# Performance work log

Hardware: AMD Instinct MI355X
Metric: run time of the kernel (lower is better)

The kernel has to match this reference:

```python
import jax, jax.numpy as jnp
import numpy as np

B, C_IN, C_OUT, H, W = 4, 256, 256, 64, 64
K, STRIDE, PAD, DIL = 3, 1, 1, 1
KK = K * K


def setup_inputs() -> dict:
    key = jax.random.key(0)
    k1, k2, k3, k4 = jax.random.split(key, 4)
    x = jax.random.normal(k1, (B, C_IN, H, W), jnp.float32)
    # offset/mask conv weight (no bias), scaled small so offsets are modest
    w_mod = jax.random.normal(k2, (3 * KK, C_IN, K, K), jnp.float32) * 0.01
    # deform conv weight (xavier-ish scale) + bias
    w_def = jax.random.normal(k3, (C_OUT, C_IN, K, K), jnp.float32) * (1.0 / np.sqrt(C_IN * KK))
    b_def = jax.random.normal(k4, (C_OUT,), jnp.float32) * 0.01
    return {"x": x, "w_mod": w_mod, "w_def": w_def, "b_def": b_def}


def _conv_nchw(x, w, stride, pad):
    return jax.lax.conv_general_dilated(
        x, w, (stride, stride), [(pad, pad), (pad, pad)],
        dimension_numbers=("NCHW", "OIHW", "NCHW"))


def _bilinear_sample(x, py, px):
    # x: [B,C,H,W]; py/px: [B,KK,Ho,Wo] absolute sample coords (zero-pad outside)
    Bn, Cc, Hh, Ww = x.shape
    y0 = jnp.floor(py)
    x0 = jnp.floor(px)
    fy = py - y0
    fx = px - x0
    y0i = y0.astype(jnp.int32)
    x0i = x0.astype(jnp.int32)
    xf = x.reshape(Bn, Cc, Hh * Ww)

    def corner(yi, xi, wgt):
        valid = (yi >= 0) & (yi < Hh) & (xi >= 0) & (xi < Ww)
        yc = jnp.clip(yi, 0, Hh - 1)
        xc = jnp.clip(xi, 0, Ww - 1)
        idx = yc * Ww + xc                      # [B,KK,Ho,Wo]
        g = jax.vmap(lambda f, i: f[:, i])(xf, idx)  # [B,C,KK,Ho,Wo]
        return g * (wgt * valid)[:, None]

    return (corner(y0i, x0i, (1 - fy) * (1 - fx))
            + corner(y0i, x0i + 1, (1 - fy) * fx)
            + corner(y0i + 1, x0i, fy * (1 - fx))
            + corner(y0i + 1, x0i + 1, fy * fx))


def reference(x, w_mod, w_def, b_def):
    # offset/mask head
    mod = _conv_nchw(x, w_mod, STRIDE, PAD)          # [B, 3*KK, Ho, Wo]
    o1, o2, mask = mod[:, :KK], mod[:, KK:2 * KK], mod[:, 2 * KK:]
    offset = jnp.concatenate([o1, o2], axis=1)        # [B, 2*KK, Ho, Wo]
    # torchvision DeformConv2d: offset channels are interleaved (y, x) pairs
    dy = offset[:, 0::2]
    dx = offset[:, 1::2]
    mask = jax.nn.sigmoid(mask)                       # [B, KK, Ho, Wo]

    Ho, Wo = mod.shape[2], mod.shape[3]
    ky, kx = jnp.meshgrid(jnp.arange(K), jnp.arange(K), indexing="ij")
    ky = ky.reshape(-1).astype(jnp.float32)
    kx = kx.reshape(-1).astype(jnp.float32)
    base_y = (jnp.arange(Ho, dtype=jnp.float32) * STRIDE - PAD)[None, :, None] + (ky * DIL)[:, None, None]  # [KK,Ho,1]
    base_x = (jnp.arange(Wo, dtype=jnp.float32) * STRIDE - PAD)[None, None, :] + (kx * DIL)[:, None, None]  # [KK,1,Wo]
    py = dy + base_y[None]                            # [B,KK,Ho,Wo]
    px = dx + base_x[None]

    sampled = _bilinear_sample(x, py, px) * mask[:, None]  # [B,C,KK,Ho,Wo]
    out = jnp.einsum("bckhw,ock->bohw", sampled, w_def.reshape(C_OUT, C_IN, KK))
    return out + b_def[None, :, None, None]
```

## Files before the change

kernel.cpp:

```cpp
#include <hip/hip_runtime.h>

typedef unsigned short u16;
typedef unsigned int u32;
typedef short bf16x8 __attribute__((ext_vector_type(8)));
typedef float f32x4 __attribute__((ext_vector_type(4)));

#define CIN 256
#define COUT 256

__device__ __forceinline__ u16 f2b(float f) {
  u32 u = __float_as_uint(f);
  u += 0x7fffu + ((u >> 16) & 1u);
  return (u16)(u >> 16);
}
__device__ __forceinline__ u32 packbf(float lo, float hi) {
  return (u32)f2b(lo) | ((u32)f2b(hi) << 16);
}
__device__ __forceinline__ u32 bil2(u32 u00, u32 u01, u32 u10, u32 u11, float4 wt) {
  float s0 = __uint_as_float(u00 << 16) * wt.x;
  s0 = fmaf(__uint_as_float(u01 << 16), wt.y, s0);
  s0 = fmaf(__uint_as_float(u10 << 16), wt.z, s0);
  s0 = fmaf(__uint_as_float(u11 << 16), wt.w, s0);
  float s1 = __uint_as_float(u00 & 0xffff0000u) * wt.x;
  s1 = fmaf(__uint_as_float(u01 & 0xffff0000u), wt.y, s1);
  s1 = fmaf(__uint_as_float(u10 & 0xffff0000u), wt.z, s1);
  s1 = fmaf(__uint_as_float(u11 & 0xffff0000u), wt.w, s1);
  return packbf(s0, s1);
}
__device__ __forceinline__ void bar() {
  asm volatile("s_waitcnt lgkmcnt(0)\n\ts_barrier" ::: "memory");
}

__global__ __launch_bounds__(256) void k_prep(
    const float* __restrict__ x, const float* __restrict__ w_mod,
    const float* __restrict__ w_def,
    u16* __restrict__ xT, u16* __restrict__ Wm2, u16* __restrict__ W2) {
  __shared__ __align__(16) char SB[9216];
  int t = threadIdx.x, g = blockIdx.x;
  if (g < 1024) {
    u16 (*T)[72] = (u16(*)[72])SB;
    int b = g >> 8, ct = (g >> 6) & 3, pt = g & 63;
    int c0 = ct << 6, pos0 = pt << 6;
    {
      int cl = t >> 2, pb = (t & 3) << 4;
      const float* p = x + (((b << 8) + c0 + cl) << 12) + pos0 + pb;
#pragma unroll
      for (int i = 0; i < 4; ++i) {
        float4 v = *(const float4*)(p + i * 4);
        int pp = pb + i * 4;
        T[pp][cl] = f2b(v.x); T[pp + 1][cl] = f2b(v.y);
        T[pp + 2][cl] = f2b(v.z); T[pp + 3][cl] = f2b(v.w);
      }
    }
    __syncthreads();
    {
      int pl = t >> 2, q = t & 3;
      u16* dst = xT + (((b << 12) + pos0 + pl) << 8) + c0 + (q << 4);
      *(uint4*)dst = *(const uint4*)&T[pl][q << 4];
      *(uint4*)(dst + 8) = *(const uint4*)&T[pl][(q << 4) + 8];
    }
  } else {
    float* L = (float*)SB;
    int gg = g - 1024;
    if (gg < 256) {
      const float* src = w_def + gg * 2304;
      for (int j = t; j < 2304; j += 256) L[j] = src[j];
      __syncthreads();
      u16* dst = W2 + gg * 2304;
      for (int j = t; j < 2304; j += 256) {
        int kk = j >> 8, c = j & 255;
        dst[j] = f2b(L[c * 9 + kk]);
      }
    } else {
      int cm = gg - 256;
      if (cm < 27) {
        const float* src = w_mod + cm * 2304;
        for (int j = t; j < 2304; j += 256) L[j] = src[j];
      }
      __syncthreads();
      u16* dst = Wm2 + cm * 2304;
      for (int j = t; j < 2304; j += 256) {
        int kk = j >> 8, c = j & 255;
        dst[j] = (cm < 27) ? f2b(L[c * 9 + kk]) : (u16)0;
      }
    }
  }
}

__global__ __launch_bounds__(512) void k_modconv(
    const u16* __restrict__ xT, const u16* __restrict__ Wm2,
    int2* __restrict__ cidx, float4* __restrict__ cwt) {
  __shared__ __align__(16) u16 As[2][2][64][72];
  __shared__ float mods2[2][32][66];
  int t = threadIdx.x;
  int l = t & 63;
  int w = t >> 6;
  int h = t >> 8;
  int wl = w & 3;
  int tg = t & 255;
  int px = tg >> 2, q = tg & 3;
  int g = blockIdx.x;
  int b = (g & 7) >> 1, y = ((g >> 3) << 1) + (g & 1);
  const u16* xTb = xT + (b << 20);
  f32x4 zero = {0.f, 0.f, 0.f, 0.f};
  f32x4 acc0 = zero, acc1 = zero;
  int ml = l & 15, kq = l >> 4;

  uint4 VA0, VA1, VB0, VB1;
  uint4 S0, S1, S2, S3, T0, T1, T2, T3;

#define MC_ISSUE_A(i, V0, V1)                                                \
  { int ch_ = h * 18 + (i); int kk_ = ch_ >> 2, c0_ = (ch_ & 3) << 6;        \
    int ky_ = kk_ / 3, kx_ = kk_ - 3 * ky_;                                  \
    int ys_ = y + ky_ - 1, xs_ = px + kx_ - 1;                               \
    V0 = make_uint4(0, 0, 0, 0); V1 = V0;                                    \
    if (ys_ >= 0 && ys_ < 64 && xs_ >= 0 && xs_ < 64) {                      \
      const u16* p_ = xTb + (((ys_ << 6) + xs_) << 8) + c0_ + (q << 4);      \
      V0 = *(const uint4*)p_; V1 = *(const uint4*)(p_ + 8);                  \
    } }

#define MC_ISSUE_B(i, R0, R1, R2, R3)                                        \
  { int ch_ = h * 18 + (i); int kk_ = ch_ >> 2, c0_ = (ch_ & 3) << 6;        \
    const u16* pw_ = Wm2 + (kk_ << 8) + c0_ + (kq << 3);                     \
    R0 = *(const uint4*)(pw_ + ml * 2304);                                   \
    R1 = *(const uint4*)(pw_ + (16 + ml) * 2304);                            \
    R2 = *(const uint4*)(pw_ + ml * 2304 + 32);                              \
    R3 = *(const uint4*)(pw_ + (16 + ml) * 2304 + 32); }

#define MC_WRITE(buf, V0, V1)                                                \
  { *(uint4*)&As[h][buf][px][q << 4] = V0;                                   \
    *(uint4*)&As[h][buf][px][(q << 4) + 8] = V1; }

#define MC_MFMA(buf, R0, R1, R2, R3)                                         \
  { bf16x8 a0_ = *(const bf16x8*)&As[h][buf][wl * 16 + ml][kq << 3];         \
    acc0 = __builtin_amdgcn_mfma_f32_16x16x32_bf16(a0_, *(const bf16x8*)&R0, acc0, 0,0,0); \
    acc1 = __builtin_amdgcn_mfma_f32_16x16x32_bf16(a0_, *(const bf16x8*)&R1, acc1, 0,0,0); \
    bf16x8 a1_ = *(const bf16x8*)&As[h][buf][wl * 16 + ml][32 + (kq << 3)];  \
    acc0 = __builtin_amdgcn_mfma_f32_16x16x32_bf16(a1_, *(const bf16x8*)&R2, acc0, 0,0,0); \
    acc1 = __builtin_amdgcn_mfma_f32_16x16x32_bf16(a1_, *(const bf16x8*)&R3, acc1, 0,0,0); }

  MC_ISSUE_A(0, VA0, VA1)
  MC_ISSUE_A(1, VB0, VB1)
  MC_ISSUE_B(0, S0, S1, S2, S3)
#pragma unroll 1
  for (int i2 = 0; i2 < 18; i2 += 2) {
    MC_WRITE(0, VA0, VA1)
    bar();
    if (i2 + 2 < 18) MC_ISSUE_A(i2 + 2, VA0, VA1)
    MC_ISSUE_B(i2 + 1, T0, T1, T2, T3)
    MC_MFMA(0, S0, S1, S2, S3)
    MC_WRITE(1, VB0, VB1)
    bar();
    if (i2 + 3 < 18) MC_ISSUE_A(i2 + 3, VB0, VB1)
    if (i2 + 2 < 18) MC_ISSUE_B(i2 + 2, S0, S1, S2, S3)
    MC_MFMA(1, T0, T1, T2, T3)
  }
#pragma unroll
  for (int r = 0; r < 4; ++r) {
    mods2[h][ml][wl * 16 + kq * 4 + r]      = acc0[r];
    mods2[h][16 + ml][wl * 16 + kq * 4 + r] = acc1[r];
  }
  __syncthreads();
  for (int i2 = t; i2 < 576; i2 += 512) {
    int kk = i2 >> 6, pxx_i = i2 & 63;
    float dy = mods2[0][2 * kk][pxx_i] + mods2[1][2 * kk][pxx_i];
    float dx = mods2[0][2 * kk + 1][pxx_i] + mods2[1][2 * kk + 1][pxx_i];
    float mv = mods2[0][18 + kk][pxx_i] + mods2[1][18 + kk][pxx_i];
    float msk = 1.f / (1.f + __expf(-mv));
    int ky = kk / 3, kx = kk - 3 * ky;
    float py  = dy + (float)(y + ky - 1);
    float pxx = dx + (float)(pxx_i + kx - 1);
    float y0f = floorf(py), x0f = floorf(pxx);
    float fy = py - y0f, fx = pxx - x0f;
    int y0 = (int)y0f, x0 = (int)x0f;
    float vy0 = (y0 >= 0 && y0 < 64) ? msk : 0.f;
    float vy1 = (y0 + 1 >= 0 && y0 + 1 < 64) ? msk : 0.f;
    float w00 = (1.f - fy) * (1.f - fx) * vy0;
    float w01 = (1.f - fy) * fx * vy0;
    float w10 = fy * (1.f - fx) * vy1;
    float w11 = fy * fx * vy1;
    int xb2 = min(max(x0, 0), 62);
    float wA0 = (xb2 == x0) ? w00 : ((xb2 == x0 + 1) ? w01 : 0.f);
    float wB0 = (xb2 + 1 == x0) ? w00 : ((xb2 + 1 == x0 + 1) ? w01 : 0.f);
    float wA1 = (xb2 == x0) ? w10 : ((xb2 == x0 + 1) ? w11 : 0.f);
    float wB1 = (xb2 + 1 == x0) ? w10 : ((xb2 + 1 == x0 + 1) ? w11 : 0.f);
    int ib0 = min(max(y0, 0), 63) * 64 + xb2;
    int ib1 = min(max(y0 + 1, 0), 63) * 64 + xb2;
    int ci = ((b * 9 + kk) << 12) + (y << 6) + pxx_i;
    cidx[ci] = make_int2(ib0, ib1);
    cwt[ci]  = make_float4(wA0, wB0, wA1, wB1);
  }
#undef MC_ISSUE_A
#undef MC_ISSUE_B
#undef MC_WRITE
#undef MC_MFMA
}

__global__ __launch_bounds__(512) void k_main(
    const u16* __restrict__ xT, const u16* __restrict__ W2,
    const float* __restrict__ b_def,
    const int2* __restrict__ cidx, const float4* __restrict__ cwt,
    float* __restrict__ out) {
  __shared__ __align__(16) u16 As[2][64][72];
  __shared__ __align__(16) int2 Cs_i[576];
  __shared__ __align__(16) float4 Cs_w[576];
  int t = threadIdx.x;
  int l = t & 63;
  int w = t >> 6;
  int g = blockIdx.x;
  int b = (g & 7) >> 1, y = ((g >> 3) << 1) + (g & 1);
  const u16* xTb = xT + (b << 20);
  int gm = t >> 3, go = t & 7;
  int ml = l & 15, kq = l >> 4;
  int nrow0 = w * 32 + ml, nrow1 = nrow0 + 16;

  f32x4 zero = {0.f, 0.f, 0.f, 0.f};
  f32x4 acc[4][2];
#pragma unroll
  for (int i = 0; i < 4; ++i) { acc[i][0] = zero; acc[i][1] = zero; }

  for (int i = t; i < 576; i += 512) {
    int kk = i >> 6, px = i & 63;
    int ci = ((b * 9 + kk) << 12) + (y << 6) + px;
    Cs_i[i] = cidx[ci];
    Cs_w[i] = cwt[ci];
  }
  bar();

  uint4 A00, A01, A02, A03; float4 wt0;
  uint4 A10, A11, A12, A13; float4 wt1;
  uint4 RA0, RA1, RA2, RA3;
  uint4 RB0, RB1, RB2, RB3;

#define ISSUE_A(chunk, a0, a1, a2, a3, wt)                                   \
  { int kk_ = (chunk) >> 2, c0_ = ((chunk) & 3) << 6;                        \
    int cI_ = (kk_ << 6) + gm;                                               \
    int2 ib_ = Cs_i[cI_];                                                    \
    wt = Cs_w[cI_];                                                          \
    const u16* p0_ = xTb + (ib_.x << 8) + c0_ + (go << 3);                   \
    const u16* p1_ = xTb + (ib_.y << 8) + c0_ + (go << 3);                   \
    a0 = *(const uint4*)p0_;  a1 = *(const uint4*)(p0_ + 256);               \
    a2 = *(const uint4*)p1_;  a3 = *(const uint4*)(p1_ + 256); }

#define ISSUE_B(chunk, R0, R1, R2, R3)                                       \
  { int kk_ = (chunk) >> 2, c0_ = ((chunk) & 3) << 6;                        \
    const u16* pw_ = W2 + (kk_ << 8) + c0_ + (kq << 3);                      \
    R0 = *(const uint4*)(pw_ + nrow0 * 2304);                                \
    R1 = *(const uint4*)(pw_ + nrow1 * 2304);                                \
    R2 = *(const uint4*)(pw_ + nrow0 * 2304 + 32);                           \
    R3 = *(const uint4*)(pw_ + nrow1 * 2304 + 32); }

#define UNPACK(CUR, a0, a1, a2, a3, wt)                                      \
  { u32 q0_ = bil2(a0.x, a1.x, a2.x, a3.x, wt);                              \
    u32 q1_ = bil2(a0.y, a1.y, a2.y, a3.y, wt);                              \
    u32 q2_ = bil2(a0.z, a1.z, a2.z, a3.z, wt);                              \
    u32 q3_ = bil2(a0.w, a1.w, a2.w, a3.w, wt);                              \
    *(uint4*)&As[CUR][gm][go << 3] = make_uint4(q0_, q1_, q2_, q3_); }

#define DOMFMA(CUR, R0, R1, R2, R3)                                          \
  { bf16x8 a0_ = *(const bf16x8*)&As[CUR][ml][kq << 3];                      \
    bf16x8 a1_ = *(const bf16x8*)&As[CUR][16 + ml][kq << 3];                 \
    bf16x8 a2_ = *(const bf16x8*)&As[CUR][32 + ml][kq << 3];                 \
    bf16x8 a3_ = *(const bf16x8*)&As[CUR][48 + ml][kq << 3];                 \
    bf16x8 b0_ = *(const bf16x8*)&R0;                                        \
    bf16x8 b1_ = *(const bf16x8*)&R1;                                        \
    acc[0][0] = __builtin_amdgcn_mfma_f32_16x16x32_bf16(a0_, b0_, acc[0][0], 0,0,0); \
    acc[1][0] = __builtin_amdgcn_mfma_f32_16x16x32_bf16(a1_, b0_, acc[1][0], 0,0,0); \
    acc[2][0] = __builtin_amdgcn_mfma_f32_16x16x32_bf16(a2_, b0_, acc[2][0], 0,0,0); \
    acc[3][0] = __builtin_amdgcn_mfma_f32_16x16x32_bf16(a3_, b0_, acc[3][0], 0,0,0); \
    acc[0][1] = __builtin_amdgcn_mfma_f32_16x16x32_bf16(a0_, b1_, acc[0][1], 0,0,0); \
    acc[1][1] = __builtin_amdgcn_mfma_f32_16x16x32_bf16(a1_, b1_, acc[1][1], 0,0,0); \
    acc[2][1] = __builtin_amdgcn_mfma_f32_16x16x32_bf16(a2_, b1_, acc[2][1], 0,0,0); \
    acc[3][1] = __builtin_amdgcn_mfma_f32_16x16x32_bf16(a3_, b1_, acc[3][1], 0,0,0); \
    a0_ = *(const bf16x8*)&As[CUR][ml][32 + (kq << 3)];                      \
    a1_ = *(const bf16x8*)&As[CUR][16 + ml][32 + (kq << 3)];                 \
    a2_ = *(const bf16x8*)&As[CUR][32 + ml][32 + (kq << 3)];                 \
    a3_ = *(const bf16x8*)&As[CUR][48 + ml][32 + (kq << 3)];                 \
    b0_ = *(const bf16x8*)&R2;                                               \
    b1_ = *(const bf16x8*)&R3;                                               \
    acc[0][0] = __builtin_amdgcn_mfma_f32_16x16x32_bf16(a0_, b0_, acc[0][0], 0,0,0); \
    acc[1][0] = __builtin_amdgcn_mfma_f32_16x16x32_bf16(a1_, b0_, acc[1][0], 0,0,0); \
    acc[2][0] = __builtin_amdgcn_mfma_f32_16x16x32_bf16(a2_, b0_, acc[2][0], 0,0,0); \
    acc[3][0] = __builtin_amdgcn_mfma_f32_16x16x32_bf16(a3_, b0_, acc[3][0], 0,0,0); \
    acc[0][1] = __builtin_amdgcn_mfma_f32_16x16x32_bf16(a0_, b1_, acc[0][1], 0,0,0); \
    acc[1][1] = __builtin_amdgcn_mfma_f32_16x16x32_bf16(a1_, b1_, acc[1][1], 0,0,0); \
    acc[2][1] = __builtin_amdgcn_mfma_f32_16x16x32_bf16(a2_, b1_, acc[2][1], 0,0,0); \
    acc[3][1] = __builtin_amdgcn_mfma_f32_16x16x32_bf16(a3_, b1_, acc[3][1], 0,0,0); }

  ISSUE_A(0, A00, A01, A02, A03, wt0)
  ISSUE_A(1, A10, A11, A12, A13, wt1)
  ISSUE_B(0, RA0, RA1, RA2, RA3)
#pragma unroll 1
  for (int c2 = 0; c2 < 36; c2 += 2) {
    UNPACK(0, A00, A01, A02, A03, wt0)
    bar();
    if (c2 + 2 < 36) ISSUE_A(c2 + 2, A00, A01, A02, A03, wt0)
    ISSUE_B(c2 + 1, RB0, RB1, RB2, RB3)
    DOMFMA(0, RA0, RA1, RA2, RA3)
    UNPACK(1, A10, A11, A12, A13, wt1)
    bar();
    if (c2 + 3 < 36) ISSUE_A(c2 + 3, A10, A11, A12, A13, wt1)
    if (c2 + 2 < 36) ISSUE_B(c2 + 2, RA0, RA1, RA2, RA3)
    DOMFMA(1, RB0, RB1, RB2, RB3)
  }

#pragma unroll
  for (int nt = 0; nt < 2; ++nt) {
    int n = w * 32 + nt * 16 + ml;
    float bias = b_def[n];
    float* op = out + (((b << 8) + n) << 12) + (y << 6);
#pragma unroll
    for (int mt = 0; mt < 4; ++mt) {
      float4 v;
      v.x = acc[mt][nt][0] + bias;
      v.y = acc[mt][nt][1] + bias;
      v.z = acc[mt][nt][2] + bias;
      v.w = acc[mt][nt][3] + bias;
      *(float4*)(op + mt * 16 + kq * 4) = v;
    }
  }
#undef ISSUE_A
#undef ISSUE_B
#undef UNPACK
#undef DOMFMA
}

extern "C" void kernel_launch(void* const* d_in, const int* in_sizes, int n_in,
                              void* d_out, int out_size, void* d_ws, size_t ws_size,
                              hipStream_t stream) {
  const float* x     = (const float*)d_in[0];
  const float* w_mod = (const float*)d_in[1];
  const float* w_def = (const float*)d_in[2];
  const float* b_def = (const float*)d_in[3];
  float* out = (float*)d_out;
  char* ws = (char*)d_ws;
  u16*    xT   = (u16*)(ws);
  u16*    W2   = (u16*)(ws + 8388608);
  u16*    Wm2  = (u16*)(ws + 8388608 + 1179648);
  int2*   cidx = (int2*)(ws + 8388608 + 1179648 + 147456);
  float4* cwt  = (float4*)(ws + 8388608 + 1179648 + 147456 + 1179648);

  hipLaunchKernelGGL(k_prep, dim3(1312), dim3(256), 0, stream, x, w_mod, w_def, xT, Wm2, W2);
  hipLaunchKernelGGL(k_modconv, dim3(256), dim3(512), 0, stream, xT, Wm2, cidx, cwt);
  hipLaunchKernelGGL(k_main, dim3(256), dim3(512), 0, stream, xT, W2, b_def, cidx, cwt, out);
}
```

Before: 159.6 us.

## Split output channels across two blocks to double grid size

Each k_main block now computes 128 output channels instead of 256 for one output row, so the grid grows from 256 to 512 blocks. Each wave holds half as many accumulators and loads half the weight fragments, and launch bounds request 4 blocks per CU for higher occupancy. The cost is that the bilinear gather and unpack of the A tile is now repeated in both channel-half blocks, doubling that work.

```diff
diff --git a/kernel.cpp b/kernel.cpp
--- a/kernel.cpp
+++ b/kernel.cpp
@@ -196,7 +196,7 @@
 #undef MC_MFMA
 }
 
-__global__ __launch_bounds__(512) void k_main(
+__global__ __launch_bounds__(512, 4) void k_main(
     const u16* __restrict__ xT, const u16* __restrict__ W2,
     const float* __restrict__ b_def,
     const int2* __restrict__ cidx, const float4* __restrict__ cwt,
@@ -208,16 +208,17 @@
   int l = t & 63;
   int w = t >> 6;
   int g = blockIdx.x;
-  int b = (g & 7) >> 1, y = ((g >> 3) << 1) + (g & 1);
+  int b = (g & 7) >> 1, nh = (g >> 3) & 1;
+  int y = ((g >> 4) << 1) + (g & 1);
   const u16* xTb = xT + (b << 20);
   int gm = t >> 3, go = t & 7;
   int ml = l & 15, kq = l >> 4;
-  int nrow0 = w * 32 + ml, nrow1 = nrow0 + 16;
+  int nrow0 = (nh << 7) + (w << 4) + ml;
 
   f32x4 zero = {0.f, 0.f, 0.f, 0.f};
-  f32x4 acc[4][2];
+  f32x4 acc[4];
 #pragma unroll
-  for (int i = 0; i < 4; ++i) { acc[i][0] = zero; acc[i][1] = zero; }
+  for (int i = 0; i < 4; ++i) acc[i] = zero;
 
   for (int i = t; i < 576; i += 512) {
     int kk = i >> 6, px = i & 63;
@@ -229,8 +230,8 @@
 
   uint4 A00, A01, A02, A03; float4 wt0;
   uint4 A10, A11, A12, A13; float4 wt1;
-  uint4 RA0, RA1, RA2, RA3;
-  uint4 RB0, RB1, RB2, RB3;
+  uint4 RA0, RA2;
+  uint4 RB0, RB2;
 
 #define ISSUE_A(chunk, a0, a1, a2, a3, wt)                                   \
   { int kk_ = (chunk) >> 2, c0_ = ((chunk) & 3) << 6;                        \
@@ -242,13 +243,11 @@
     a0 = *(const uint4*)p0_;  a1 = *(const uint4*)(p0_ + 256);               \
     a2 = *(const uint4*)p1_;  a3 = *(const uint4*)(p1_ + 256); }
 
-#define ISSUE_B(chunk, R0, R1, R2, R3)                                       \
+#define ISSUE_B(chunk, R0, R2)                                               \
   { int kk_ = (chunk) >> 2, c0_ = ((chunk) & 3) << 6;                        \
     const u16* pw_ = W2 + (kk_ << 8) + c0_ + (kq << 3);                      \
     R0 = *(const uint4*)(pw_ + nrow0 * 2304);                                \
-    R1 = *(const uint4*)(pw_ + nrow1 * 2304);                                \
-    R2 = *(const uint4*)(pw_ + nrow0 * 2304 + 32);                           \
-    R3 = *(const uint4*)(pw_ + nrow1 * 2304 + 32); }
+    R2 = *(const uint4*)(pw_ + nrow0 * 2304 + 32); }
 
 #define UNPACK(CUR, a0, a1, a2, a3, wt)                                      \
   { u32 q0_ = bil2(a0.x, a1.x, a2.x, a3.x, wt);                              \
@@ -257,65 +256,54 @@
     u32 q3_ = bil2(a0.w, a1.w, a2.w, a3.w, wt);                              \
     *(uint4*)&As[CUR][gm][go << 3] = make_uint4(q0_, q1_, q2_, q3_); }
 
-#define DOMFMA(CUR, R0, R1, R2, R3)                                          \
+#define DOMFMA(CUR, R0, R2)                                                  \
   { bf16x8 a0_ = *(const bf16x8*)&As[CUR][ml][kq << 3];                      \
     bf16x8 a1_ = *(const bf16x8*)&As[CUR][16 + ml][kq << 3];                 \
     bf16x8 a2_ = *(const bf16x8*)&As[CUR][32 + ml][kq << 3];                 \
     bf16x8 a3_ = *(const bf16x8*)&As[CUR][48 + ml][kq << 3];                 \
     bf16x8 b0_ = *(const bf16x8*)&R0;                                        \
-    bf16x8 b1_ = *(const bf16x8*)&R1;                                        \
-    acc[0][0] = __builtin_amdgcn_mfma_f32_16x16x32_bf16(a0_, b0_, acc[0][0], 0,0,0); \
-    acc[1][0] = __builtin_amdgcn_mfma_f32_16x16x32_bf16(a1_, b0_, acc[1][0], 0,0,0); \
-    acc[2][0] = __builtin_amdgcn_mfma_f32_16x16x32_bf16(a2_, b0_, acc[2][0], 0,0,0); \
-    acc[3][0] = __builtin_amdgcn_mfma_f32_16x16x32_bf16(a3_, b0_, acc[3][0], 0,0,0); \
-    acc[0][1] = __builtin_amdgcn_mfma_f32_16x16x32_bf16(a0_, b1_, acc[0][1], 0,0,0); \
-    acc[1][1] = __builtin_amdgcn_mfma_f32_16x16x32_bf16(a1_, b1_, acc[1][1], 0,0,0); \
-    acc[2][1] = __builtin_amdgcn_mfma_f32_16x16x32_bf16(a2_, b1_, acc[2][1], 0,0,0); \
-    acc[3][1] = __builtin_amdgcn_mfma_f32_16x16x32_bf16(a3_, b1_, acc[3][1], 0,0,0); \
+    acc[0] = __builtin_amdgcn_mfma_f32_16x16x32_bf16(a0_, b0_, acc[0], 0,0,0); \
+    acc[1] = __builtin_amdgcn_mfma_f32_16x16x32_bf16(a1_, b0_, acc[1], 0,0,0); \
+    acc[2] = __builtin_amdgcn_mfma_f32_16x16x32_bf16(a2_, b0_, acc[2], 0,0,0); \
+    acc[3] = __builtin_amdgcn_mfma_f32_16x16x32_bf16(a3_, b0_, acc[3], 0,0,0); \
     a0_ = *(const bf16x8*)&As[CUR][ml][32 + (kq << 3)];                      \
     a1_ = *(const bf16x8*)&As[CUR][16 + ml][32 + (kq << 3)];                 \
     a2_ = *(const bf16x8*)&As[CUR][32 + ml][32 + (kq << 3)];                 \
     a3_ = *(const bf16x8*)&As[CUR][48 + ml][32 + (kq << 3)];                 \
     b0_ = *(const bf16x8*)&R2;                                               \
-    b1_ = *(const bf16x8*)&R3;                                               \
-    acc[0][0] = __builtin_amdgcn_mfma_f32_16x16x32_bf16(a0_, b0_, acc[0][0], 0,0,0); \
-    acc[1][0] = __builtin_amdgcn_mfma_f32_16x16x32_bf16(a1_, b0_, acc[1][0], 0,0,0); \
-    acc[2][0] = __builtin_amdgcn_mfma_f32_16x16x32_bf16(a2_, b0_, acc[2][0], 0,0,0); \
-    acc[3][0] = __builtin_amdgcn_mfma_f32_16x16x32_bf16(a3_, b0_, acc[3][0], 0,0,0); \
-    acc[0][1] = __builtin_amdgcn_mfma_f32_16x16x32_bf16(a0_, b1_, acc[0][1], 0,0,0); \
-    acc[1][1] = __builtin_amdgcn_mfma_f32_16x16x32_bf16(a1_, b1_, acc[1][1], 0,0,0); \
-    acc[2][1] = __builtin_amdgcn_mfma_f32_16x16x32_bf16(a2_, b1_, acc[2][1], 0,0,0); \
-    acc[3][1] = __builtin_amdgcn_mfma_f32_16x16x32_bf16(a3_, b1_, acc[3][1], 0,0,0); }
+    acc[0] = __builtin_amdgcn_mfma_f32_16x16x32_bf16(a0_, b0_, acc[0], 0,0,0); \
+    acc[1] = __builtin_amdgcn_mfma_f32_16x16x32_bf16(a1_, b0_, acc[1], 0,0,0); \
+    acc[2] = __builtin_amdgcn_mfma_f32_16x16x32_bf16(a2_, b0_, acc[2], 0,0,0); \
+    acc[3] = __builtin_amdgcn_mfma_f32_16x16x32_bf16(a3_, b0_, acc[3], 0,0,0); }
 
   ISSUE_A(0, A00, A01, A02, A03, wt0)
   ISSUE_A(1, A10, A11, A12, A13, wt1)
-  ISSUE_B(0, RA0, RA1, RA2, RA3)
+  ISSUE_B(0, RA0, RA2)
 #pragma unroll 1
   for (int c2 = 0; c2 < 36; c2 += 2) {
     UNPACK(0, A00, A01, A02, A03, wt0)
     bar();
     if (c2 + 2 < 36) ISSUE_A(c2 + 2, A00, A01, A02, A03, wt0)
-    ISSUE_B(c2 + 1, RB0, RB1, RB2, RB3)
-    DOMFMA(0, RA0, RA1, RA2, RA3)
+    ISSUE_B(c2 + 1, RB0, RB2)
+    DOMFMA(0, RA0, RA2)
     UNPACK(1, A10, A11, A12, A13, wt1)
     bar();
     if (c2 + 3 < 36) ISSUE_A(c2 + 3, A10, A11, A12, A13, wt1)
-    if (c2 + 2 < 36) ISSUE_B(c2 + 2, RA0, RA1, RA2, RA3)
-    DOMFMA(1, RB0, RB1, RB2, RB3)
-  }
-
-#pragma unroll
-  for (int nt = 0; nt < 2; ++nt) {
-    int n = w * 32 + nt * 16 + ml;
+    if (c2 + 2 < 36) ISSUE_B(c2 + 2, RA0, RA2)
+    DOMFMA(1, RB0, RB2)
+  }
+
+  {
+    int n = nrow0;
     float bias = b_def[n];
     float* op = out + (((b << 8) + n) << 12) + (y << 6);
 #pragma unroll
     for (int mt = 0; mt < 4; ++mt) {
       float4 v;
-      v.x = acc[mt][nt][0] + bias;
-      v.y = acc[mt][nt][1] + bias;
-      v.z = acc[mt][nt][2] + bias;
-      v.w = acc[mt][nt][3] + bias;
+      v.x = acc[mt][0] + bias;
+      v.y = acc[mt][1] + bias;
+      v.z = acc[mt][2] + bias;
+      v.w = acc[mt][3] + bias;
       *(float4*)(op + mt * 16 + kq * 4) = v;
     }
   }
@@ -342,5 +330,5 @@
 
   hipLaunchKernelGGL(k_prep, dim3(1312), dim3(256), 0, stream, x, w_mod, w_def, xT, Wm2, W2);
   hipLaunchKernelGGL(k_modconv, dim3(256), dim3(512), 0, stream, xT, Wm2, cidx, cwt);
-  hipLaunchKernelGGL(k_main, dim3(256), dim3(512), 0, stream, xT, W2, b_def, cidx, cwt, out);
-}
+  hipLaunchKernelGGL(k_main, dim3(512), dim3(512), 0, stream, xT, W2, b_def, cidx, cwt, out);
+}
```

Result: no change. 162.0 us (+1.5%).
